# Kernel optimization log

Measured on AMD Instinct MI355X. Metric: run time of the kernel, lower is better.

The kernel has to match this reference:

```python
import jax, jax.numpy as jnp
import numpy as np

HEADS = 8
DIM_HEAD = 64
QUERY_DIM = 512
INNER_DIM = HEADS * DIM_HEAD  # 512


def setup_inputs() -> dict:
    key = jax.random.key(0)
    ks = jax.random.split(key, 6)
    B, S = 2, 4096
    hidden_states = jax.random.normal(ks[0], (B, S, QUERY_DIM), dtype=jnp.float32)
    # torch nn.Linear stores weight as [out, in]; y = x @ W.T (+ b)
    std = 0.02
    Wq = jax.random.normal(ks[1], (INNER_DIM, QUERY_DIM), dtype=jnp.float32) * std
    Wk = jax.random.normal(ks[2], (INNER_DIM, QUERY_DIM), dtype=jnp.float32) * std
    Wv = jax.random.normal(ks[3], (INNER_DIM, QUERY_DIM), dtype=jnp.float32) * std
    Wo = jax.random.normal(ks[4], (QUERY_DIM, INNER_DIM), dtype=jnp.float32) * std
    bo = jax.random.normal(ks[5], (QUERY_DIM,), dtype=jnp.float32) * std
    return {"hidden_states": hidden_states, "Wq": Wq, "Wk": Wk, "Wv": Wv, "Wo": Wo, "bo": bo}


def reference(hidden_states, Wq, Wk, Wv, Wo, bo):
    B, S, D = hidden_states.shape
    H, dh = HEADS, DIM_HEAD
    # QKV projections (no bias, per bias=False)
    q = jnp.einsum("bsd,ed->bse", hidden_states, Wq)
    k = jnp.einsum("bsd,ed->bse", hidden_states, Wk)
    v = jnp.einsum("bsd,ed->bse", hidden_states, Wv)
    # split heads: [B, S, H*dh] -> [B, H, S, dh]
    q = q.reshape(B, S, H, dh).transpose(0, 2, 1, 3)
    k = k.reshape(B, S, H, dh).transpose(0, 2, 1, 3)
    v = v.reshape(B, S, H, dh).transpose(0, 2, 1, 3)
    scale = 1.0 / jnp.sqrt(jnp.asarray(dh, dtype=q.dtype))
    scores = jnp.einsum("bhqd,bhkd->bhqk", q, k) * scale
    attn = jax.nn.softmax(scores, axis=-1)
    out = jnp.einsum("bhqk,bhkd->bhqd", attn, v)
    # merge heads back: [B, H, S, dh] -> [B, S, H*dh]
    out = out.transpose(0, 2, 1, 3).reshape(B, S, H * dh)
    # output projection (Linear with bias); dropout p=0.0 is identity
    return jnp.einsum("bse,de->bsd", out, Wo) + bo
```

## Files before the change

### kernel.cpp

```cpp
#include <hip/hip_runtime.h>
#include <stdint.h>

typedef _Float16 half_t;
typedef _Float16 half8 __attribute__((ext_vector_type(8)));
typedef __fp16 fp16x2 __attribute__((ext_vector_type(2)));
typedef float floatx4 __attribute__((ext_vector_type(4)));
typedef float floatx16 __attribute__((ext_vector_type(16)));
typedef unsigned int uint;
typedef unsigned int uint4v __attribute__((ext_vector_type(4)));

#define LOG2E 1.4426950408889634f

__device__ __forceinline__ void gload_lds16(const void* g, void* l) {
  __builtin_amdgcn_global_load_lds(
      (__attribute__((address_space(1))) void*)(uintptr_t)g,
      (__attribute__((address_space(3))) void*)(uintptr_t)l, 16, 0, 0);
}

__device__ __forceinline__ int swz64(int b)  { return b ^ (((b >> 7) & 3) << 4); }
__device__ __forceinline__ int swz128(int b) { return b ^ (((b >> 7) & 7) << 4); }

__device__ __forceinline__ uint pkrtz(float a, float b) {
  union { fp16x2 h; uint u; } cv;
  cv.h = __builtin_amdgcn_cvt_pkrtz(a, b);
  return cv.u;
}
__device__ __forceinline__ void pl32swap(uint &x, uint &y) {
  asm("v_permlane32_swap_b32 %0, %1" : "+v"(x), "+v"(y));
}
__device__ __forceinline__ half8 as_h8(uint4v v) {
  union { uint4v u; half8 h; } c; c.u = v; return c.h;
}

__global__ void cvt_x_kernel(const float* __restrict__ X, half_t* __restrict__ X16) {
  int i = (blockIdx.x * 256 + threadIdx.x) * 8;
  float4 u = *(const float4*)(X + i);
  float4 v = *(const float4*)(X + i + 4);
  half8 o = {(half_t)u.x, (half_t)u.y, (half_t)u.z, (half_t)u.w,
             (half_t)v.x, (half_t)v.y, (half_t)v.z, (half_t)v.w};
  *(half8*)(X16 + i) = o;
}

__global__ void cvt_w_kernel(const float* __restrict__ Wq, const float* __restrict__ Wk,
                             const float* __restrict__ Wv, const float* __restrict__ Wo,
                             half_t* __restrict__ W16) {
  int i = blockIdx.x * 256 + threadIdx.x;
  int widx = i >> 15;
  int j = (i & 32767) * 8;
  const float* src = (widx == 0) ? Wq : (widx == 1) ? Wk : (widx == 2) ? Wv : Wo;
  float sc = (widx == 0) ? 0.125f * LOG2E : 1.0f;
  float4 u = *(const float4*)(src + j);
  float4 v = *(const float4*)(src + j + 4);
  half8 o = {(half_t)(u.x * sc), (half_t)(u.y * sc), (half_t)(u.z * sc), (half_t)(u.w * sc),
             (half_t)(v.x * sc), (half_t)(v.y * sc), (half_t)(v.z * sc), (half_t)(v.w * sc)};
  *(half8*)(W16 + widx * 262144 + j) = o;
}

template <int MODE>
__global__ __launch_bounds__(256) void gemm_nt(
    const half_t* __restrict__ A, const half_t* __restrict__ B0,
    const half_t* __restrict__ B1, half_t* __restrict__ outh,
    half_t* __restrict__ outh2, float* __restrict__ outf,
    const float* __restrict__ bias) {
  __shared__ __attribute__((aligned(16))) half_t As[128 * 32];
  __shared__ __attribute__((aligned(16))) half_t Bs[128 * 32];

  const int tid = threadIdx.x;
  const int w = tid >> 6, l = tid & 63, g = l >> 4, c = l & 15;
  const int wr = w >> 1, wc = w & 1;
  const int bidx = blockIdx.x;

  int rt, ct;
  const half_t *Ab, *Bb;
  if (MODE == 0) {
    rt = bidx >> 3; ct = bidx & 7;
    Ab = A + (size_t)rt * 128 * 512;
    Bb = ((ct < 4) ? B0 : B1) + (size_t)(ct & 3) * 128 * 512;
  } else if (MODE == 1) {
    rt = bidx >> 6; ct = bidx & 63;
    Ab = A + (size_t)rt * 128 * 512;
    Bb = B0 + (size_t)ct * 128 * 512;
  } else {
    rt = bidx >> 2; ct = bidx & 3;
    Ab = A + (size_t)rt * 128 * 512;
    Bb = B0 + (size_t)ct * 128 * 512;
  }

  const floatx4 fzero = {0.f, 0.f, 0.f, 0.f};
  floatx4 acc[4][4];
#pragma unroll
  for (int m = 0; m < 4; ++m)
#pragma unroll
    for (int n = 0; n < 4; ++n) acc[m][n] = fzero;

  for (int kt = 0; kt < 16; ++kt) {
    __syncthreads();
#pragma unroll
    for (int i = 0; i < 2; ++i) {
      int rel = i * 4096 + tid * 16;
      int lg = swz64(rel);
      int row = lg >> 6, inner = (lg & 63) >> 1;
      gload_lds16(Ab + (size_t)row * 512 + kt * 32 + inner, As + (rel >> 1));
      gload_lds16(Bb + (size_t)row * 512 + kt * 32 + inner, Bs + (rel >> 1));
    }
    __syncthreads();
    half8 a[4], b[4];
#pragma unroll
    for (int m = 0; m < 4; ++m)
      a[m] = *(const half8*)&As[swz64(((wr * 64 + m * 16 + c) << 6) + (g << 4)) >> 1];
#pragma unroll
    for (int n = 0; n < 4; ++n)
      b[n] = *(const half8*)&Bs[swz64(((wc * 64 + n * 16 + c) << 6) + (g << 4)) >> 1];
#pragma unroll
    for (int m = 0; m < 4; ++m)
#pragma unroll
      for (int n = 0; n < 4; ++n)
        acc[m][n] = __builtin_amdgcn_mfma_f32_16x16x32_f16(a[m], b[n], acc[m][n], 0, 0, 0);
  }

  const int r0 = wr * 64, c0 = wc * 64;
  if (MODE == 0) {
    half_t* O = ((ct < 4) ? outh : outh2) + (size_t)rt * 128 * 512 + (size_t)(ct & 3) * 128;
#pragma unroll
    for (int m = 0; m < 4; ++m)
#pragma unroll
      for (int j = 0; j < 4; ++j)
#pragma unroll
        for (int n = 0; n < 4; ++n)
          O[(size_t)(r0 + m * 16 + g * 4 + j) * 512 + c0 + n * 16 + c] = (half_t)acc[m][n][j];
  } else if (MODE == 1) {
    half_t* O = outh + (size_t)(ct >> 5) * 2097152 + (size_t)(ct & 31) * 128;
#pragma unroll
    for (int m = 0; m < 4; ++m)
#pragma unroll
      for (int j = 0; j < 4; ++j)
#pragma unroll
        for (int n = 0; n < 4; ++n)
          O[(size_t)(rt * 128 + r0 + m * 16 + g * 4 + j) * 4096 + c0 + n * 16 + c] =
              (half_t)acc[m][n][j];
  } else {
    float* O = outf + (size_t)rt * 128 * 512 + ct * 128;
    float bv[4];
#pragma unroll
    for (int n = 0; n < 4; ++n) bv[n] = bias[ct * 128 + c0 + n * 16 + c];
#pragma unroll
    for (int m = 0; m < 4; ++m)
#pragma unroll
      for (int j = 0; j < 4; ++j)
#pragma unroll
        for (int n = 0; n < 4; ++n)
          O[(size_t)(r0 + m * 16 + g * 4 + j) * 512 + c0 + n * 16 + c] = acc[m][n][j] + bv[n];
  }
}

__global__ __launch_bounds__(256, 2) void attn_kernel(
    const half_t* __restrict__ Q16, const half_t* __restrict__ K16,
    const half_t* __restrict__ Vt, half_t* __restrict__ O16) {
  __shared__ __attribute__((aligned(16))) char smem[33 * 1024];
  half_t* kb_lds = (half_t*)smem;
  half_t* vb_lds = (half_t*)(smem + 16384);

  const int tid = threadIdx.x;
  const int w = tid >> 6, l = tid & 63, lo = l & 31, h = l >> 5;
  const int kw = w >> 1, qw = w & 1;
  const int bid = (blockIdx.x & 7) * 64 + (blockIdx.x >> 3);
  const int bh = bid >> 5, qt = bid & 31;
  const int b = bh >> 3, hh = bh & 7;

  const half_t* Qb = Q16 + (size_t)(b * 4096 + qt * 128 + qw * 64) * 512 + hh * 64;
  const half_t* Kb = K16 + (size_t)b * 4096 * 512 + hh * 64;
  const half_t* Vb = Vt + (size_t)bh * 262144;
  half_t* Ob = O16 + (size_t)(b * 4096 + qt * 128 + qw * 64) * 512 + hh * 64;

  half8 qa[2][4];
#pragma unroll
  for (int qm = 0; qm < 2; ++qm)
#pragma unroll
    for (int ks = 0; ks < 4; ++ks)
      qa[qm][ks] = *(const half8*)(Qb + (size_t)(qm * 32 + lo) * 512 + ks * 16 + h * 8);

  floatx16 acc[2][2];
#pragma unroll
  for (int qm = 0; qm < 2; ++qm)
#pragma unroll
    for (int dn = 0; dn < 2; ++dn)
#pragma unroll
      for (int r = 0; r < 16; ++r) acc[qm][dn][r] = 0.f;
  float lf[2] = {0.f, 0.f};

  auto stage = [&](int buf, int t) {
#pragma unroll
    for (int i = 0; i < 2; ++i) {
      int rel = i * 4096 + tid * 16;
      int lg = swz128(rel);
      int row = lg >> 7, inner = (lg & 127) >> 1;
      gload_lds16(Kb + (size_t)(t * 64 + row) * 512 + inner,
                  kb_lds + buf * 4096 + (rel >> 1));
      gload_lds16(Vb + (size_t)row * 4096 + t * 64 + inner,
                  vb_lds + buf * 4096 + (rel >> 1));
    }
  };

  stage(0, 0);
  int cur = 0;

  for (int t = 0; t < 64; ++t) {
    __syncthreads();
    if (t < 63) stage(cur ^ 1, t + 1);

    floatx16 s[2];
#pragma unroll
    for (int qm = 0; qm < 2; ++qm)
#pragma unroll
      for (int r = 0; r < 16; ++r) s[qm][r] = 0.f;

#pragma unroll
    for (int ks = 0; ks < 4; ++ks) {
      int byte = ((kw * 32 + lo) << 7) + (ks << 5) + (h << 4);
      half8 ka = *(const half8*)&kb_lds[cur * 4096 + (swz128(byte) >> 1)];
#pragma unroll
      for (int qm = 0; qm < 2; ++qm)
        s[qm] = __builtin_amdgcn_mfma_f32_32x32x16_f16(ka, qa[qm][ks], s[qm], 0, 0, 0);
    }

    uint4v pa[2][2];
#pragma unroll
    for (int qm = 0; qm < 2; ++qm) {
      float psum = 0.f;
#pragma unroll
      for (int r = 0; r < 16; ++r) {
        float e = __builtin_amdgcn_exp2f(s[qm][r]);
        s[qm][r] = e;
        psum += e;
      }
      lf[qm] += psum;
#pragma unroll
      for (int ksb = 0; ksb < 2; ++ksb) {
        uint x0 = pkrtz(s[qm][8 * ksb + 0], s[qm][8 * ksb + 1]);
        uint x1 = pkrtz(s[qm][8 * ksb + 2], s[qm][8 * ksb + 3]);
        uint y0 = pkrtz(s[qm][8 * ksb + 4], s[qm][8 * ksb + 5]);
        uint y1 = pkrtz(s[qm][8 * ksb + 6], s[qm][8 * ksb + 7]);
        pl32swap(x0, y0);
        pl32swap(x1, y1);
        pa[qm][ksb] = (uint4v){x0, x1, y0, y1};
      }
    }

#pragma unroll
    for (int dn = 0; dn < 2; ++dn)
#pragma unroll
      for (int ks = 0; ks < 2; ++ks) {
        int byte = ((dn * 32 + lo) << 7) + ((kw * 32 + ks * 16 + h * 8) << 1);
        half8 vb = *(const half8*)&vb_lds[cur * 4096 + (swz128(byte) >> 1)];
#pragma unroll
        for (int qm = 0; qm < 2; ++qm)
          acc[qm][dn] =
              __builtin_amdgcn_mfma_f32_32x32x16_f16(as_h8(pa[qm][ks]), vb, acc[qm][dn], 0, 0, 0);
      }

    cur ^= 1;
  }

#pragma unroll
  for (int qm = 0; qm < 2; ++qm) lf[qm] += __shfl_xor(lf[qm], 32);

  float* red = (float*)smem;
  float* redl = (float*)(smem + 32768);

  __syncthreads();
  if (kw == 1) {
#pragma unroll
    for (int qm = 0; qm < 2; ++qm) {
      redl[(qw * 2 + qm) * 64 + l] = lf[qm];
#pragma unroll
      for (int dn = 0; dn < 2; ++dn)
#pragma unroll
        for (int r = 0; r < 16; ++r)
          red[((((qw * 2 + qm) * 2 + dn) * 16) + r) * 64 + l] = acc[qm][dn][r];
    }
  }
  __syncthreads();
  if (kw == 0) {
    float inv[2];
#pragma unroll
    for (int qm = 0; qm < 2; ++qm)
      inv[qm] = 1.0f / (lf[qm] + redl[(qw * 2 + qm) * 64 + l]);
#pragma unroll
    for (int qm = 0; qm < 2; ++qm)
#pragma unroll
      for (int r = 0; r < 16; ++r) {
        int ro = (r & 3) + 8 * (r >> 2) + 4 * h;
        float iv = __shfl(inv[qm], ro);
#pragma unroll
        for (int dn = 0; dn < 2; ++dn) {
          float o = (acc[qm][dn][r] + red[((((qw * 2 + qm) * 2 + dn) * 16) + r) * 64 + l]) * iv;
          Ob[(size_t)(qm * 32 + ro) * 512 + dn * 32 + lo] = (half_t)o;
        }
      }
  }
}

extern "C" void kernel_launch(void* const* d_in, const int* in_sizes, int n_in,
                              void* d_out, int out_size, void* d_ws, size_t ws_size,
                              hipStream_t stream) {
  const float* X  = (const float*)d_in[0];
  const float* Wq = (const float*)d_in[1];
  const float* Wk = (const float*)d_in[2];
  const float* Wv = (const float*)d_in[3];
  const float* Wo = (const float*)d_in[4];
  const float* bo = (const float*)d_in[5];
  float* out = (float*)d_out;

  char* ws = (char*)d_ws;
  half_t* X16  = (half_t*)(ws);
  half_t* W16  = (half_t*)(ws + 8388608);
  half_t* Q16  = (half_t*)(ws + 10485760);
  half_t* K16  = (half_t*)(ws + 18874368);
  half_t* VtW  = (half_t*)(ws + 27262976);
  half_t* O16  = (half_t*)(ws + 35651584);
  half_t* Wq16 = W16;
  half_t* Wk16 = W16 + 262144;
  half_t* Wv16 = W16 + 524288;
  half_t* Wo16 = W16 + 786432;

  cvt_x_kernel<<<2048, 256, 0, stream>>>(X, X16);
  cvt_w_kernel<<<512, 256, 0, stream>>>(Wq, Wk, Wv, Wo, W16);
  gemm_nt<0><<<512, 256, 0, stream>>>(X16, Wq16, Wk16, Q16, K16, nullptr, nullptr);
  gemm_nt<1><<<256, 256, 0, stream>>>(Wv16, X16, nullptr, VtW, nullptr, nullptr, nullptr);
  attn_kernel<<<512, 256, 0, stream>>>(Q16, K16, VtW, O16);
  gemm_nt<2><<<256, 256, 0, stream>>>(O16, Wo16, nullptr, nullptr, nullptr, out, bo);
}
```

Baseline: 135.7 us.

## Double attention block size to split key tiles across two wave groups

The attention kernel now runs 512 threads per block. Two groups of four waves each process alternating 64-key tiles from a pair staged together in LDS, which halves the number of loop iterations and barriers per group. Partial accumulators and row sums from the second group are reduced into the first through LDS before the existing split-key reduction. This raises parallelism per block and doubles LDS use to about 66KB, which may limit occupancy and adds an extra reduction step.

```diff
diff --git a/kernel.cpp b/kernel.cpp
--- a/kernel.cpp
+++ b/kernel.cpp
@@ -153,16 +153,17 @@
   }
 }
 
-__global__ __launch_bounds__(256, 2) void attn_kernel(
+__global__ __launch_bounds__(512, 2) void attn_kernel(
     const half_t* __restrict__ Q16, const half_t* __restrict__ K16,
     const half_t* __restrict__ Vt, half_t* __restrict__ O16) {
-  __shared__ __attribute__((aligned(16))) char smem[33 * 1024];
+  __shared__ __attribute__((aligned(16))) char smem[67584];
   half_t* kb_lds = (half_t*)smem;
-  half_t* vb_lds = (half_t*)(smem + 16384);
+  half_t* vb_lds = (half_t*)(smem + 32768);
 
   const int tid = threadIdx.x;
   const int w = tid >> 6, l = tid & 63, lo = l & 31, h = l >> 5;
-  const int kw = w >> 1, qw = w & 1;
+  const int tp = w >> 2, w4 = w & 3;
+  const int kw = w4 >> 1, qw = w4 & 1;
   const int bid = (blockIdx.x & 7) * 64 + (blockIdx.x >> 3);
   const int bh = bid >> 5, qt = bid & 31;
   const int b = bh >> 3, hh = bh & 7;
@@ -188,25 +189,26 @@
       for (int r = 0; r < 16; ++r) acc[qm][dn][r] = 0.f;
   float lf[2] = {0.f, 0.f};
 
-  auto stage = [&](int buf, int t) {
-#pragma unroll
-    for (int i = 0; i < 2; ++i) {
-      int rel = i * 4096 + tid * 16;
-      int lg = swz128(rel);
-      int row = lg >> 7, inner = (lg & 127) >> 1;
-      gload_lds16(Kb + (size_t)(t * 64 + row) * 512 + inner,
-                  kb_lds + buf * 4096 + (rel >> 1));
-      gload_lds16(Vb + (size_t)row * 4096 + t * 64 + inner,
-                  vb_lds + buf * 4096 + (rel >> 1));
+  auto stage2 = [&](int pair, int t0) {
+    int rel = tid * 16;
+    int lg = swz128(rel);
+    int row = lg >> 7, inner = (lg & 127) >> 1;
+#pragma unroll
+    for (int sl = 0; sl < 2; ++sl) {
+      gload_lds16(Kb + (size_t)((t0 + sl) * 64 + row) * 512 + inner,
+                  kb_lds + pair * 8192 + sl * 4096 + (rel >> 1));
+      gload_lds16(Vb + (size_t)row * 4096 + (t0 + sl) * 64 + inner,
+                  vb_lds + pair * 8192 + sl * 4096 + (rel >> 1));
     }
   };
 
-  stage(0, 0);
-  int cur = 0;
-
-  for (int t = 0; t < 64; ++t) {
-    __syncthreads();
-    if (t < 63) stage(cur ^ 1, t + 1);
+  stage2(0, 0);
+
+  for (int j = 0; j < 32; ++j) {
+    __syncthreads();
+    if (j < 31) stage2((j + 1) & 1, 2 * (j + 1));
+    const half_t* kt = kb_lds + (j & 1) * 8192 + tp * 4096;
+    const half_t* vt = vb_lds + (j & 1) * 8192 + tp * 4096;
 
     floatx16 s[2];
 #pragma unroll
@@ -217,7 +219,7 @@
 #pragma unroll
     for (int ks = 0; ks < 4; ++ks) {
       int byte = ((kw * 32 + lo) << 7) + (ks << 5) + (h << 4);
-      half8 ka = *(const half8*)&kb_lds[cur * 4096 + (swz128(byte) >> 1)];
+      half8 ka = *(const half8*)&kt[swz128(byte) >> 1];
 #pragma unroll
       for (int qm = 0; qm < 2; ++qm)
         s[qm] = __builtin_amdgcn_mfma_f32_32x32x16_f16(ka, qa[qm][ks], s[qm], 0, 0, 0);
@@ -251,24 +253,44 @@
 #pragma unroll
       for (int ks = 0; ks < 2; ++ks) {
         int byte = ((dn * 32 + lo) << 7) + ((kw * 32 + ks * 16 + h * 8) << 1);
-        half8 vb = *(const half8*)&vb_lds[cur * 4096 + (swz128(byte) >> 1)];
+        half8 vb = *(const half8*)&vt[swz128(byte) >> 1];
 #pragma unroll
         for (int qm = 0; qm < 2; ++qm)
           acc[qm][dn] =
               __builtin_amdgcn_mfma_f32_32x32x16_f16(as_h8(pa[qm][ks]), vb, acc[qm][dn], 0, 0, 0);
       }
-
-    cur ^= 1;
+  }
+
+  float* red = (float*)smem;
+  float* redl = (float*)(smem + 65536);
+
+#pragma unroll
+  for (int qm = 0; qm < 2; ++qm) {
+    __syncthreads();
+    if (tp == 1) {
+      redl[qm * 256 + w4 * 64 + l] = lf[qm];
+#pragma unroll
+      for (int dn = 0; dn < 2; ++dn)
+#pragma unroll
+        for (int r = 0; r < 16; ++r)
+          red[((w4 * 2 + dn) * 16 + r) * 64 + l] = acc[qm][dn][r];
+    }
+    __syncthreads();
+    if (tp == 0) {
+      lf[qm] += redl[qm * 256 + w4 * 64 + l];
+#pragma unroll
+      for (int dn = 0; dn < 2; ++dn)
+#pragma unroll
+        for (int r = 0; r < 16; ++r)
+          acc[qm][dn][r] += red[((w4 * 2 + dn) * 16 + r) * 64 + l];
+    }
   }
 
 #pragma unroll
   for (int qm = 0; qm < 2; ++qm) lf[qm] += __shfl_xor(lf[qm], 32);
 
-  float* red = (float*)smem;
-  float* redl = (float*)(smem + 32768);
-
   __syncthreads();
-  if (kw == 1) {
+  if (tp == 0 && kw == 1) {
 #pragma unroll
     for (int qm = 0; qm < 2; ++qm) {
       redl[(qw * 2 + qm) * 64 + l] = lf[qm];
@@ -280,7 +302,7 @@
     }
   }
   __syncthreads();
-  if (kw == 0) {
+  if (tp == 0 && kw == 0) {
     float inv[2];
 #pragma unroll
     for (int qm = 0; qm < 2; ++qm)
@@ -327,6 +349,6 @@
   cvt_w_kernel<<<512, 256, 0, stream>>>(Wq, Wk, Wv, Wo, W16);
   gemm_nt<0><<<512, 256, 0, stream>>>(X16, Wq16, Wk16, Q16, K16, nullptr, nullptr);
   gemm_nt<1><<<256, 256, 0, stream>>>(Wv16, X16, nullptr, VtW, nullptr, nullptr, nullptr);
-  attn_kernel<<<512, 256, 0, stream>>>(Q16, K16, VtW, O16);
+  attn_kernel<<<512, 512, 0, stream>>>(Q16, K16, VtW, O16);
   gemm_nt<2><<<256, 256, 0, stream>>>(O16, Wo16, nullptr, nullptr, nullptr, out, bo);
 }
```

Result: slower. 139.3 us (+2.7%).

## Deepen attention K/V LDS pipeline to four slots with explicit vmcnt waits

Applied to the files above, without the earlier changes.

Replaces the double-buffered K/V staging with a four-slot ring that keeps three tiles in flight, using explicit s_waitcnt vmcnt and raw barriers instead of __syncthreads. It also raises wave priority around the MFMA sections with s_setprio. The goal is to hide global-to-LDS load latency better. The cost is doubling LDS to about 65KB per block, which may limit occupancy to fewer blocks per CU than the launch bounds request, and the hand-counted vmcnt values must match the issued load counts.

```diff
diff --git a/kernel.cpp b/kernel.cpp
--- a/kernel.cpp
+++ b/kernel.cpp
@@ -156,9 +156,9 @@
 __global__ __launch_bounds__(256, 2) void attn_kernel(
     const half_t* __restrict__ Q16, const half_t* __restrict__ K16,
     const half_t* __restrict__ Vt, half_t* __restrict__ O16) {
-  __shared__ __attribute__((aligned(16))) char smem[33 * 1024];
+  __shared__ __attribute__((aligned(16))) char smem[66560];
   half_t* kb_lds = (half_t*)smem;
-  half_t* vb_lds = (half_t*)(smem + 16384);
+  half_t* vb_lds = (half_t*)(smem + 32768);
 
   const int tid = threadIdx.x;
   const int w = tid >> 6, l = tid & 63, lo = l & 31, h = l >> 5;
@@ -188,25 +188,22 @@
       for (int r = 0; r < 16; ++r) acc[qm][dn][r] = 0.f;
   float lf[2] = {0.f, 0.f};
 
-  auto stage = [&](int buf, int t) {
+  auto stage = [&](int slot, int t) {
 #pragma unroll
     for (int i = 0; i < 2; ++i) {
       int rel = i * 4096 + tid * 16;
       int lg = swz128(rel);
       int row = lg >> 7, inner = (lg & 127) >> 1;
       gload_lds16(Kb + (size_t)(t * 64 + row) * 512 + inner,
-                  kb_lds + buf * 4096 + (rel >> 1));
+                  kb_lds + slot * 4096 + (rel >> 1));
       gload_lds16(Vb + (size_t)row * 4096 + t * 64 + inner,
-                  vb_lds + buf * 4096 + (rel >> 1));
+                  vb_lds + slot * 4096 + (rel >> 1));
     }
   };
 
-  stage(0, 0);
-  int cur = 0;
-
-  for (int t = 0; t < 64; ++t) {
-    __syncthreads();
-    if (t < 63) stage(cur ^ 1, t + 1);
+  auto compute = [&](int slot) {
+    const half_t* kt = kb_lds + slot * 4096;
+    const half_t* vt = vb_lds + slot * 4096;
 
     floatx16 s[2];
 #pragma unroll
@@ -214,14 +211,16 @@
 #pragma unroll
       for (int r = 0; r < 16; ++r) s[qm][r] = 0.f;
 
+    __builtin_amdgcn_s_setprio(1);
 #pragma unroll
     for (int ks = 0; ks < 4; ++ks) {
       int byte = ((kw * 32 + lo) << 7) + (ks << 5) + (h << 4);
-      half8 ka = *(const half8*)&kb_lds[cur * 4096 + (swz128(byte) >> 1)];
+      half8 ka = *(const half8*)&kt[swz128(byte) >> 1];
 #pragma unroll
       for (int qm = 0; qm < 2; ++qm)
         s[qm] = __builtin_amdgcn_mfma_f32_32x32x16_f16(ka, qa[qm][ks], s[qm], 0, 0, 0);
     }
+    __builtin_amdgcn_s_setprio(0);
 
     uint4v pa[2][2];
 #pragma unroll
@@ -246,26 +245,50 @@
       }
     }
 
+    __builtin_amdgcn_s_setprio(1);
 #pragma unroll
     for (int dn = 0; dn < 2; ++dn)
 #pragma unroll
       for (int ks = 0; ks < 2; ++ks) {
         int byte = ((dn * 32 + lo) << 7) + ((kw * 32 + ks * 16 + h * 8) << 1);
-        half8 vb = *(const half8*)&vb_lds[cur * 4096 + (swz128(byte) >> 1)];
+        half8 vb = *(const half8*)&vt[swz128(byte) >> 1];
 #pragma unroll
         for (int qm = 0; qm < 2; ++qm)
           acc[qm][dn] =
               __builtin_amdgcn_mfma_f32_32x32x16_f16(as_h8(pa[qm][ks]), vb, acc[qm][dn], 0, 0, 0);
       }
-
-    cur ^= 1;
-  }
+    __builtin_amdgcn_s_setprio(0);
+  };
+
+  stage(0, 0);
+  stage(1, 1);
+  stage(2, 2);
+
+  for (int t = 0; t < 61; ++t) {
+    asm volatile("s_waitcnt vmcnt(8)" ::: "memory");
+    __builtin_amdgcn_s_barrier();
+    __builtin_amdgcn_sched_barrier(0);
+    stage((t + 3) & 3, t + 3);
+    compute(t & 3);
+  }
+  asm volatile("s_waitcnt vmcnt(8)" ::: "memory");
+  __builtin_amdgcn_s_barrier();
+  __builtin_amdgcn_sched_barrier(0);
+  compute(1);
+  asm volatile("s_waitcnt vmcnt(4)" ::: "memory");
+  __builtin_amdgcn_s_barrier();
+  __builtin_amdgcn_sched_barrier(0);
+  compute(2);
+  asm volatile("s_waitcnt vmcnt(0)" ::: "memory");
+  __builtin_amdgcn_s_barrier();
+  __builtin_amdgcn_sched_barrier(0);
+  compute(3);
 
 #pragma unroll
   for (int qm = 0; qm < 2; ++qm) lf[qm] += __shfl_xor(lf[qm], 32);
 
   float* red = (float*)smem;
-  float* redl = (float*)(smem + 32768);
+  float* redl = (float*)(smem + 65536);
 
   __syncthreads();
   if (kw == 1) {
```

New measurement: 137.7 us. No clear change (+1.5%).

## Software-pipeline attention loop with 5-slot LDS ring and QK/softmax/PV overlap

Applied to the files above, without the earlier changes.

Replaces the double-buffered K/V staging with a 5-slot LDS ring that prefetches three tiles ahead, using explicit vmcnt waits plus barriers. The loop is software-pipelined so the QK MFMAs for tile t+1 are interleaved with the exp2/pack of tile t's scores, followed by the PV MFMAs at raised wave priority. The aim is to hide global-load latency and overlap transcendental work with matrix ops. LDS usage grows to 80KB per block, which may reduce occupancy below the 2 blocks per CU requested by launch bounds.

```diff
diff --git a/kernel.cpp b/kernel.cpp
--- a/kernel.cpp
+++ b/kernel.cpp
@@ -31,6 +31,11 @@
 __device__ __forceinline__ half8 as_h8(uint4v v) {
   union { uint4v u; half8 h; } c; c.u = v; return c.h;
 }
+
+#define WAITB(N)                                          \
+  asm volatile("s_waitcnt vmcnt(" #N ")" ::: "memory");   \
+  __builtin_amdgcn_s_barrier();                           \
+  __builtin_amdgcn_sched_barrier(0);
 
 __global__ void cvt_x_kernel(const float* __restrict__ X, half_t* __restrict__ X16) {
   int i = (blockIdx.x * 256 + threadIdx.x) * 8;
@@ -156,9 +161,9 @@
 __global__ __launch_bounds__(256, 2) void attn_kernel(
     const half_t* __restrict__ Q16, const half_t* __restrict__ K16,
     const half_t* __restrict__ Vt, half_t* __restrict__ O16) {
-  __shared__ __attribute__((aligned(16))) char smem[33 * 1024];
+  __shared__ __attribute__((aligned(16))) char smem[81920];
   half_t* kb_lds = (half_t*)smem;
-  half_t* vb_lds = (half_t*)(smem + 16384);
+  half_t* vb_lds = (half_t*)(smem + 40960);
 
   const int tid = threadIdx.x;
   const int w = tid >> 6, l = tid & 63, lo = l & 31, h = l >> 5;
@@ -188,77 +193,134 @@
       for (int r = 0; r < 16; ++r) acc[qm][dn][r] = 0.f;
   float lf[2] = {0.f, 0.f};
 
-  auto stage = [&](int buf, int t) {
+  floatx16 fz16;
+#pragma unroll
+  for (int r = 0; r < 16; ++r) fz16[r] = 0.f;
+
+  auto stage = [&](int slot, int t) {
 #pragma unroll
     for (int i = 0; i < 2; ++i) {
       int rel = i * 4096 + tid * 16;
       int lg = swz128(rel);
       int row = lg >> 7, inner = (lg & 127) >> 1;
       gload_lds16(Kb + (size_t)(t * 64 + row) * 512 + inner,
-                  kb_lds + buf * 4096 + (rel >> 1));
+                  kb_lds + slot * 4096 + (rel >> 1));
       gload_lds16(Vb + (size_t)row * 4096 + t * 64 + inner,
-                  vb_lds + buf * 4096 + (rel >> 1));
-    }
-  };
-
-  stage(0, 0);
-  int cur = 0;
-
-  for (int t = 0; t < 64; ++t) {
-    __syncthreads();
-    if (t < 63) stage(cur ^ 1, t + 1);
-
-    floatx16 s[2];
-#pragma unroll
-    for (int qm = 0; qm < 2; ++qm)
-#pragma unroll
-      for (int r = 0; r < 16; ++r) s[qm][r] = 0.f;
-
+                  vb_lds + slot * 4096 + (rel >> 1));
+    }
+  };
+
+  auto qk_only = [&](int slotQK, floatx16 (&sNew)[2]) {
+    const half_t* kt = kb_lds + slotQK * 4096;
 #pragma unroll
     for (int ks = 0; ks < 4; ++ks) {
       int byte = ((kw * 32 + lo) << 7) + (ks << 5) + (h << 4);
-      half8 ka = *(const half8*)&kb_lds[cur * 4096 + (swz128(byte) >> 1)];
-#pragma unroll
-      for (int qm = 0; qm < 2; ++qm)
-        s[qm] = __builtin_amdgcn_mfma_f32_32x32x16_f16(ka, qa[qm][ks], s[qm], 0, 0, 0);
-    }
-
-    uint4v pa[2][2];
-#pragma unroll
-    for (int qm = 0; qm < 2; ++qm) {
-      float psum = 0.f;
-#pragma unroll
-      for (int r = 0; r < 16; ++r) {
-        float e = __builtin_amdgcn_exp2f(s[qm][r]);
-        s[qm][r] = e;
-        psum += e;
+      half8 ka = *(const half8*)&kt[swz128(byte) >> 1];
+      if (ks == 0) {
+        sNew[0] = __builtin_amdgcn_mfma_f32_32x32x16_f16(ka, qa[0][0], fz16, 0, 0, 0);
+        sNew[1] = __builtin_amdgcn_mfma_f32_32x32x16_f16(ka, qa[1][0], fz16, 0, 0, 0);
+      } else {
+        sNew[0] = __builtin_amdgcn_mfma_f32_32x32x16_f16(ka, qa[0][ks], sNew[0], 0, 0, 0);
+        sNew[1] = __builtin_amdgcn_mfma_f32_32x32x16_f16(ka, qa[1][ks], sNew[1], 0, 0, 0);
       }
-      lf[qm] += psum;
-#pragma unroll
-      for (int ksb = 0; ksb < 2; ++ksb) {
-        uint x0 = pkrtz(s[qm][8 * ksb + 0], s[qm][8 * ksb + 1]);
-        uint x1 = pkrtz(s[qm][8 * ksb + 2], s[qm][8 * ksb + 3]);
-        uint y0 = pkrtz(s[qm][8 * ksb + 4], s[qm][8 * ksb + 5]);
-        uint y1 = pkrtz(s[qm][8 * ksb + 6], s[qm][8 * ksb + 7]);
-        pl32swap(x0, y0);
-        pl32swap(x1, y1);
-        pa[qm][ksb] = (uint4v){x0, x1, y0, y1};
-      }
-    }
-
+    }
+  };
+
+  auto chunk = [&](floatx16 (&sOld)[2], int qm, int ksb, uint4v (&pa)[2][2]) {
+    float e[8];
+    float ps = 0.f;
+#pragma unroll
+    for (int j = 0; j < 8; ++j) {
+      e[j] = __builtin_amdgcn_exp2f(sOld[qm][8 * ksb + j]);
+      ps += e[j];
+    }
+    lf[qm] += ps;
+    uint x0 = pkrtz(e[0], e[1]), x1 = pkrtz(e[2], e[3]);
+    uint y0 = pkrtz(e[4], e[5]), y1 = pkrtz(e[6], e[7]);
+    pl32swap(x0, y0);
+    pl32swap(x1, y1);
+    pa[qm][ksb] = (uint4v){x0, x1, y0, y1};
+  };
+
+  auto pv = [&](int slotPV, uint4v (&pa)[2][2]) {
+    const half_t* vt = vb_lds + slotPV * 4096;
+    __builtin_amdgcn_s_setprio(1);
 #pragma unroll
     for (int dn = 0; dn < 2; ++dn)
 #pragma unroll
       for (int ks = 0; ks < 2; ++ks) {
         int byte = ((dn * 32 + lo) << 7) + ((kw * 32 + ks * 16 + h * 8) << 1);
-        half8 vb = *(const half8*)&vb_lds[cur * 4096 + (swz128(byte) >> 1)];
+        half8 vb = *(const half8*)&vt[swz128(byte) >> 1];
 #pragma unroll
         for (int qm = 0; qm < 2; ++qm)
           acc[qm][dn] =
               __builtin_amdgcn_mfma_f32_32x32x16_f16(as_h8(pa[qm][ks]), vb, acc[qm][dn], 0, 0, 0);
       }
-
-    cur ^= 1;
+    __builtin_amdgcn_s_setprio(0);
+  };
+
+  auto full_round = [&](int slotQK, int slotPV, floatx16 (&sOld)[2], floatx16 (&sNew)[2]) {
+    const half_t* kt = kb_lds + slotQK * 4096;
+    uint4v pa[2][2];
+#pragma unroll
+    for (int ks = 0; ks < 4; ++ks) {
+      int byte = ((kw * 32 + lo) << 7) + (ks << 5) + (h << 4);
+      half8 ka = *(const half8*)&kt[swz128(byte) >> 1];
+      if (ks == 0) {
+        sNew[0] = __builtin_amdgcn_mfma_f32_32x32x16_f16(ka, qa[0][0], fz16, 0, 0, 0);
+        sNew[1] = __builtin_amdgcn_mfma_f32_32x32x16_f16(ka, qa[1][0], fz16, 0, 0, 0);
+      } else {
+        sNew[0] = __builtin_amdgcn_mfma_f32_32x32x16_f16(ka, qa[0][ks], sNew[0], 0, 0, 0);
+        sNew[1] = __builtin_amdgcn_mfma_f32_32x32x16_f16(ka, qa[1][ks], sNew[1], 0, 0, 0);
+      }
+      chunk(sOld, ks >> 1, ks & 1, pa);
+    }
+    pv(slotPV, pa);
+  };
+
+  floatx16 sA[2], sB[2];
+
+  stage(0, 0);
+  stage(1, 1);
+  stage(2, 2);
+
+  WAITB(8)
+  stage(3, 3);
+  qk_only(0, sA);
+
+  int sStage = 4, sQK = 1, sPV = 0;
+  for (int r = 1; r <= 60; r += 2) {
+    WAITB(8)
+    stage(sStage, r + 3);
+    full_round(sQK, sPV, sA, sB);
+    sStage = (sStage == 4) ? 0 : sStage + 1;
+    sQK = (sQK == 4) ? 0 : sQK + 1;
+    sPV = (sPV == 4) ? 0 : sPV + 1;
+
+    WAITB(8)
+    stage(sStage, r + 4);
+    full_round(sQK, sPV, sB, sA);
+    sStage = (sStage == 4) ? 0 : sStage + 1;
+    sQK = (sQK == 4) ? 0 : sQK + 1;
+    sPV = (sPV == 4) ? 0 : sPV + 1;
+  }
+  WAITB(8)
+  full_round(sQK, sPV, sA, sB);
+  sQK = (sQK == 4) ? 0 : sQK + 1;
+  sPV = (sPV == 4) ? 0 : sPV + 1;
+  WAITB(4)
+  full_round(sQK, sPV, sB, sA);
+  sQK = (sQK == 4) ? 0 : sQK + 1;
+  sPV = (sPV == 4) ? 0 : sPV + 1;
+  WAITB(0)
+  full_round(sQK, sPV, sA, sB);
+  sPV = (sPV == 4) ? 0 : sPV + 1;
+
+  {
+    uint4v pa[2][2];
+#pragma unroll
+    for (int ks = 0; ks < 4; ++ks) chunk(sB, ks >> 1, ks & 1, pa);
+    pv(sPV, pa);
   }
 
 #pragma unroll
```

Result: no change. 134.2 us (-1.1%).
